# Optimization experiments

Measured on AMD Instinct MI355X. Metric: run time of the kernel, lower is better.

The kernel has to match this reference:

```python
import jax, jax.numpy as jnp
import numpy as np

NPOINT = 1024
RADIUS = 0.15
NSAMPLE = 32
BN_EPS = 1e-5


def farthest_point_sample(xyz, npoint):
    # xyz: [B, N, 3] -> idx [B, npoint]
    B, N, _ = xyz.shape

    def step(carry, _):
        dmin, far = carry
        cent = jnp.take_along_axis(xyz, far[:, None, None], axis=1)  # [B,1,3]
        d = jnp.sum((xyz - cent) ** 2, axis=-1)                      # [B,N]
        dmin = jnp.minimum(dmin, d)
        nxt = jnp.argmax(dmin, axis=-1).astype(jnp.int32)
        return (dmin, nxt), far

    init = (jnp.full((B, N), 1e10, xyz.dtype), jnp.zeros((B,), jnp.int32))
    _, idx = jax.lax.scan(step, init, None, length=npoint)
    return idx.T  # [B, npoint]


def ball_query(radius, nsample, xyz, new_xyz):
    # xyz: [B,N,3], new_xyz: [B,S,3] -> idx [B,S,nsample]
    B, S, _ = new_xyz.shape
    N = xyz.shape[1]
    sqr = jnp.sum((new_xyz[:, :, None, :] - xyz[:, None, :, :]) ** 2, axis=-1)  # [B,S,N]
    ar = jnp.broadcast_to(jnp.arange(N, dtype=jnp.int32), (B, S, N))
    gidx = jnp.where(sqr > radius * radius, N, ar)
    gidx = jnp.sort(gidx, axis=-1)[:, :, :nsample]
    first = gidx[:, :, :1]
    return jnp.where(gidx == N, first, gidx)


def setup_inputs() -> dict:
    key = jax.random.key(0)
    ks = jax.random.split(key, 8)
    B, N, Cin, Cmlp, Cout = 8, 4096, 64, 128, 256
    xyz = jax.random.uniform(ks[0], (B, N, 3), dtype=jnp.float32)
    t = jax.random.normal(ks[1], (B, 128), dtype=jnp.float32)
    points = jax.random.normal(ks[2], (B, N, Cin), dtype=jnp.float32)
    W1 = jax.random.normal(ks[3], (Cin, Cmlp), dtype=jnp.float32) / np.sqrt(Cin)
    b1 = jnp.zeros((Cmlp,), jnp.float32)
    Wc = jax.random.normal(ks[4], (Cmlp, Cout), dtype=jnp.float32) / np.sqrt(Cmlp)
    bc = jnp.zeros((Cout,), jnp.float32)
    gamma = jnp.ones((Cout,), jnp.float32)
    beta = jnp.zeros((Cout,), jnp.float32)
    return {"xyz": xyz, "t": t, "points": points, "W1": W1, "b1": b1,
            "Wc": Wc, "bc": bc, "gamma": gamma, "beta": beta}


def reference(xyz, t, points, W1, b1, Wc, bc, gamma, beta):
    # t (time embedding) is unused in the visible (truncated) forward body.
    B, N, _ = xyz.shape
    # 1) farthest point sampling -> centers
    fps_idx = farthest_point_sample(xyz, NPOINT)                     # [B,S]
    new_xyz = jnp.take_along_axis(xyz, fps_idx[:, :, None], axis=1)  # [B,S,3]
    # 2) radius ball-query grouping
    gidx = ball_query(RADIUS, NSAMPLE, xyz, new_xyz)                 # [B,S,ns]
    # 3) pointwise MLP on features, then group (gather)
    feats = points @ W1 + b1                                          # [B,N,Cmlp]
    grouped = jax.vmap(lambda f, i: f[i])(feats, gidx)                # [B,S,ns,Cmlp]
    # 4) GroupConv: 1x1 conv + BatchNorm(train stats) + ReLU
    h = jnp.einsum('bsnc,co->bsno', grouped, Wc) + bc                 # [B,S,ns,Cout]
    mean = jnp.mean(h, axis=(0, 1, 2))
    var = jnp.var(h, axis=(0, 1, 2))
    h = jax.nn.relu((h - mean) / jnp.sqrt(var + BN_EPS) * gamma + beta)
    # 5) max-pool over neighborhood
    new_points = jnp.max(h, axis=2)                                   # [B,S,Cout]
    return new_points
```

## Files before the change

### kernel.cpp

```cpp
#include <hip/hip_runtime.h>
#include <stdint.h>

#define BN 8
#define NPT 4096
#define NS 1024
#define KS 32
#define CIN 64
#define CMID 128
#define COUT 256
#define NGRP (BN*NS)

typedef short bf16x8 __attribute__((ext_vector_type(8)));
typedef float f32x4 __attribute__((ext_vector_type(4)));

__device__ __forceinline__ float bf2f(unsigned short u){
  union { unsigned int i; float f; } v; v.i = ((unsigned int)u) << 16; return v.f;
}
__device__ __forceinline__ unsigned short f2bf(float f){
  union { float f; unsigned int i; } v; v.f = f;
  unsigned int r = (v.i + 0x7fffu + ((v.i >> 16) & 1u)) >> 16;
  return (unsigned short)r;
}
__device__ __forceinline__ uint32_t pack2(float a, float b){
  return (uint32_t)f2bf(a) | ((uint32_t)f2bf(b) << 16);
}
__device__ __forceinline__ float ldf(const void* p, size_t i, bool isbf){
  return isbf ? bf2f(((const unsigned short*)p)[i]) : ((const float*)p)[i];
}
__device__ __forceinline__ bool detect_bf(const void* gamma){
  return ((const unsigned int*)gamma)[0] == 0x3F803F80u;
}

template<int CTRL>
__device__ __forceinline__ unsigned long long dpp_rot_u64(unsigned long long x){
  int lo = (int)(unsigned int)(x & 0xFFFFFFFFull);
  int hi = (int)(unsigned int)(x >> 32);
  int nlo = __builtin_amdgcn_update_dpp(0, lo, CTRL, 0xF, 0xF, true);
  int nhi = __builtin_amdgcn_update_dpp(0, hi, CTRL, 0xF, 0xF, true);
  return ((unsigned long long)(unsigned int)nhi << 32) | (unsigned int)nlo;
}
__device__ __forceinline__ unsigned long long u64max(unsigned long long a, unsigned long long b){
  return a > b ? a : b;
}

__global__ __launch_bounds__(512, 2)
void k_front(const void* __restrict__ xyz,
             const void* __restrict__ points,
             const void* __restrict__ W1,
             const void* __restrict__ Wc,
             const void* __restrict__ gamma,
             float* __restrict__ newxyz,
             unsigned short* __restrict__ featsb,
             unsigned short* __restrict__ wct,
             float* __restrict__ ps, float* __restrict__ pq, int nbins)
{
  int tid = threadIdx.x;
  int bid = blockIdx.x;
  bool isbf = detect_bf(gamma);
  __shared__ __align__(16) char smem[49152];
  __shared__ unsigned long long wk[2][8];

  if (bid < 8){
    float* sx = (float*)smem;
    float* sy = sx + NPT;
    float* sz = sy + NPT;
    size_t xb = (size_t)bid*NPT*3;
    for (int i=tid; i<NPT; i+=512){
      size_t p = xb + (size_t)i*3;
      sx[i]=ldf(xyz,p,isbf); sy[i]=ldf(xyz,p+1,isbf); sz[i]=ldf(xyz,p+2,isbf);
    }
    __syncthreads();
    int base = tid*8;
    float px0,px1,px2,px3,px4,px5,px6,px7;
    float py0,py1,py2,py3,py4,py5,py6,py7;
    float pz0,pz1,pz2,pz3,pz4,pz5,pz6,pz7;
    float dm0,dm1,dm2,dm3,dm4,dm5,dm6,dm7;
#define FPS_LOAD(k) px##k=sx[base+k]; py##k=sy[base+k]; pz##k=sz[base+k]; dm##k=1e10f;
    FPS_LOAD(0) FPS_LOAD(1) FPS_LOAD(2) FPS_LOAD(3)
    FPS_LOAD(4) FPS_LOAD(5) FPS_LOAD(6) FPS_LOAD(7)
#undef FPS_LOAD
    float cx=sx[0], cy=sy[0], cz=sz[0];
    if (tid==0){ float* o = newxyz + (size_t)bid*NS*3; o[0]=cx; o[1]=cy; o[2]=cz; }
    int lane = tid & 63, wv = tid >> 6;
    unsigned int lo0 = (unsigned int)(4095 - base);
    for (int it=1; it<NS; ++it){
      int par = it & 1;
#define FPS_STEP(k) { float dx=__fsub_rn(px##k,cx), dy=__fsub_rn(py##k,cy), dz=__fsub_rn(pz##k,cz); \
  float d=__fadd_rn(__fadd_rn(__fmul_rn(dx,dx),__fmul_rn(dy,dy)),__fmul_rn(dz,dz)); \
  dm##k=fminf(dm##k,d); }
      FPS_STEP(0) FPS_STEP(1) FPS_STEP(2) FPS_STEP(3)
      FPS_STEP(4) FPS_STEP(5) FPS_STEP(6) FPS_STEP(7)
#undef FPS_STEP
      bool c01 = dm1 > dm0; float v01 = c01?dm1:dm0; int i01 = c01?1:0;
      bool c23 = dm3 > dm2; float v23 = c23?dm3:dm2; int i23 = c23?3:2;
      bool c45 = dm5 > dm4; float v45 = c45?dm5:dm4; int i45 = c45?5:4;
      bool c67 = dm7 > dm6; float v67 = c67?dm7:dm6; int i67 = c67?7:6;
      bool ca = v23 > v01; float va = ca?v23:v01; int ia = ca?i23:i01;
      bool cb = v67 > v45; float vb = cb?v67:v45; int ib = cb?i67:i45;
      bool cc = vb  > va;  float vm = cc?vb:va;   int ir = cc?ib:ia;
      unsigned long long key =
        ((unsigned long long)__float_as_uint(vm) << 32) | (unsigned int)(lo0 - ir);
      key = u64max(key, dpp_rot_u64<0x121>(key));
      key = u64max(key, dpp_rot_u64<0x122>(key));
      key = u64max(key, dpp_rot_u64<0x124>(key));
      key = u64max(key, dpp_rot_u64<0x128>(key));
      key = u64max(key, __shfl_xor(key, 16, 64));
      key = u64max(key, __shfl_xor(key, 32, 64));
      if (lane == 0) wk[par][wv] = key;
      __syncthreads();
      const unsigned long long* w8 = wk[par];
      unsigned long long k0 =
        u64max(u64max(u64max(w8[0],w8[1]), u64max(w8[2],w8[3])),
               u64max(u64max(w8[4],w8[5]), u64max(w8[6],w8[7])));
      int widx = 4095 - (int)(k0 & 0xFFFFFFFFull);
      cx = sx[widx]; cy = sy[widx]; cz = sz[widx];
      if (tid==0){ float* o = newxyz + ((size_t)bid*NS + it)*3; o[0]=cx; o[1]=cy; o[2]=cz; }
    }
  } else if (bid == 8){
    for (int i=tid; i<CMID*COUT; i+=512){
      int k = i >> 8, n = i & 255;
      unsigned short w = isbf ? ((const unsigned short*)Wc)[i] : f2bf(((const float*)Wc)[i]);
      wct[(size_t)n*CMID + k] = w;
    }
    if (nbins != NGRP){
      for (int i=tid; i<COUT*nbins; i+=512){ ps[i]=0.f; pq[i]=0.f; }
    }
  } else {
    float* w1s = (float*)smem;
    float* pts = (float*)(smem + 32768);
    int rb = bid - 9;
    int r0g = rb*64;
    for (int i=tid; i<CIN*CMID; i+=512) w1s[i] = ldf(W1, i, isbf);
    for (int i=tid; i<64*CIN; i+=512)   pts[i] = ldf(points, (size_t)r0g*CIN + i, isbf);
    __syncthreads();
    int o0 = (tid & 15) * 8, r0 = (tid >> 4) * 2;
    float acc0[8]={0,0,0,0,0,0,0,0}, acc1[8]={0,0,0,0,0,0,0,0};
    for (int c=0;c<CIN;c++){
      float a0 = pts[r0*CIN + c], a1 = pts[(r0+1)*CIN + c];
      const float* wr = &w1s[c*CMID + o0];
      #pragma unroll
      for (int j=0;j<8;j++){ acc0[j] = fmaf(a0, wr[j], acc0[j]); acc1[j] = fmaf(a1, wr[j], acc1[j]); }
    }
    unsigned short* f0 = featsb + ((size_t)(r0g + r0))*CMID + o0;
    uint4 u;
    u.x=pack2(acc0[0],acc0[1]); u.y=pack2(acc0[2],acc0[3]); u.z=pack2(acc0[4],acc0[5]); u.w=pack2(acc0[6],acc0[7]);
    *(uint4*)f0 = u;
    u.x=pack2(acc1[0],acc1[1]); u.y=pack2(acc1[2],acc1[3]); u.z=pack2(acc1[4],acc1[5]); u.w=pack2(acc1[6],acc1[7]);
    *(uint4*)(f0 + CMID) = u;
  }
}

__global__ __launch_bounds__(256)
void k_ballq(const void* __restrict__ xyz,
             const void* __restrict__ gamma,
             const float* __restrict__ newxyz,
             int* __restrict__ gidx)
{
  __shared__ float sp[NPT*3];
  __shared__ int slots[4][KS];
  int tid = threadIdx.x;
  bool isbf = detect_bf(gamma);
  int cb = blockIdx.x * 64;
  int b = cb >> 10;
  size_t xb = (size_t)b*NPT*3;
  for (int i=tid; i<NPT*3; i+=256) sp[i] = ldf(xyz, xb + i, isbf);
  __syncthreads();
  int lane = tid & 63, wv = tid >> 6;
  const float rr = (float)(0.15*0.15);
  for (int j=0; j<16; ++j){
    int cid = cb + wv*16 + j;
    const float* cc = newxyz + (size_t)cid*3;
    float cx=cc[0], cy=cc[1], cz=cc[2];
    int cnt = 0;
    for (int ch=0; ch<64; ++ch){
      int p = ch*64 + lane;
      float dx=__fsub_rn(sp[p*3],cx), dy=__fsub_rn(sp[p*3+1],cy), dz=__fsub_rn(sp[p*3+2],cz);
      float d=__fadd_rn(__fadd_rn(__fmul_rn(dx,dx),__fmul_rn(dy,dy)),__fmul_rn(dz,dz));
      bool in = !(d > rr);
      unsigned long long mk = __ballot(in);
      int pos = cnt + __popcll(mk & ((1ull<<lane) - 1ull));
      if (in && pos < KS) slots[wv][pos] = p;
      cnt += __popcll(mk);
      if (cnt >= KS) break;
    }
    int total = cnt < KS ? cnt : KS;
    if (lane < KS){
      int v = (lane < total) ? slots[wv][lane] : slots[wv][0];
      gidx[(size_t)cid*KS + lane] = v;
    }
  }
}

__global__ __launch_bounds__(256)
void k_group(const unsigned short* __restrict__ featsb,
             const unsigned short* __restrict__ wct,
             const int* __restrict__ gidx,
             const void* __restrict__ gamma,
             float* __restrict__ ps, float* __restrict__ pq,
             const float* __restrict__ av, const float* __restrict__ cv,
             float* __restrict__ hM,
             void* __restrict__ out, int mode, int nbins)
{
  int tid = threadIdx.x;
  int bs  = blockIdx.x;
  __shared__ unsigned short g[32][136];
  __shared__ int gi[KS];
  if (tid < KS) gi[tid] = gidx[(size_t)bs*KS + tid];
  __syncthreads();
  {
    int r = tid >> 3, sg = tid & 7;
    const unsigned short* src = featsb + ((size_t)(bs>>10)*NPT + gi[r])*CMID + sg*16;
    uint4 v0 = *(const uint4*)src;
    uint4 v1 = *(const uint4*)(src + 8);
    *(uint4*)(&g[r][sg*16])     = v0;
    *(uint4*)(&g[r][sg*16 + 8]) = v1;
  }
  __syncthreads();
  int lane = tid & 63, wv = tid >> 6;
  int m = lane & 15, quad = lane >> 4;
  f32x4 acc[2][4];
  #pragma unroll
  for (int a=0;a<2;a++)
    #pragma unroll
    for (int b2=0;b2<4;b2++) acc[a][b2] = (f32x4){0.f,0.f,0.f,0.f};
  int n0 = wv * 64;
  #pragma unroll
  for (int k0=0; k0<CMID; k0+=32){
    bf16x8 a0 = *(const bf16x8*)(&g[m][k0 + quad*8]);
    bf16x8 a1 = *(const bf16x8*)(&g[16 + m][k0 + quad*8]);
    #pragma unroll
    for (int nt=0; nt<4; nt++){
      int n = n0 + nt*16 + m;
      bf16x8 bb = *(const bf16x8*)(wct + (size_t)n*CMID + k0 + quad*8);
      acc[0][nt] = __builtin_amdgcn_mfma_f32_16x16x32_bf16(a0, bb, acc[0][nt], 0, 0, 0);
      acc[1][nt] = __builtin_amdgcn_mfma_f32_16x16x32_bf16(a1, bb, acc[1][nt], 0, 0, 0);
    }
  }
  if (mode == 2){
    #pragma unroll
    for (int nt=0; nt<4; nt++){
      float s=0.f, q=0.f, hx=-3.402823466e38f;
      #pragma unroll
      for (int mt=0; mt<2; mt++)
        #pragma unroll
        for (int rg=0; rg<4; rg++){ float h = acc[mt][nt][rg]; s += h; q += h*h; hx = fmaxf(hx,h); }
      s += __shfl_xor(s,16,64); q += __shfl_xor(q,16,64); hx = fmaxf(hx, __shfl_xor(hx,16,64));
      s += __shfl_xor(s,32,64); q += __shfl_xor(q,32,64); hx = fmaxf(hx, __shfl_xor(hx,32,64));
      if (quad == 0){
        int o = n0 + nt*16 + m;
        ps[(size_t)o*NGRP + bs] = s;
        pq[(size_t)o*NGRP + bs] = q;
        hM[(size_t)bs*COUT + o] = hx;
      }
    }
  } else if (mode == 0){
    #pragma unroll
    for (int nt=0; nt<4; nt++){
      float s=0.f, q=0.f;
      #pragma unroll
      for (int mt=0; mt<2; mt++)
        #pragma unroll
        for (int rg=0; rg<4; rg++){ float h = acc[mt][nt][rg]; s += h; q += h*h; }
      s += __shfl_xor(s,16,64); q += __shfl_xor(q,16,64);
      s += __shfl_xor(s,32,64); q += __shfl_xor(q,32,64);
      if (quad == 0){
        int o = n0 + nt*16 + m;
        atomicAdd(&ps[(size_t)o*nbins + (bs & (nbins-1))], s);
        atomicAdd(&pq[(size_t)o*nbins + (bs & (nbins-1))], q);
      }
    }
  } else {
    bool isbf = detect_bf(gamma);
    #pragma unroll
    for (int nt=0; nt<4; nt++){
      int o = n0 + nt*16 + m;
      float a = av[o], c = cv[o];
      float v = 0.f;
      #pragma unroll
      for (int mt=0; mt<2; mt++)
        #pragma unroll
        for (int rg=0; rg<4; rg++){ v = fmaxf(v, acc[mt][nt][rg]*a + c); }
      v = fmaxf(v, __shfl_xor(v,16,64));
      v = fmaxf(v, __shfl_xor(v,32,64));
      if (quad == 0){
        size_t oi = (size_t)bs*COUT + o;
        if (isbf) ((unsigned short*)out)[oi] = f2bf(v);
        else      ((float*)out)[oi] = v;
      }
    }
  }
}

__global__ __launch_bounds__(256)
void k_bnprep(const float* __restrict__ ps, const float* __restrict__ pq,
              const void* __restrict__ gamma, const void* __restrict__ beta,
              float* __restrict__ av, float* __restrict__ cv, int nbins)
{
  int tid = threadIdx.x, o = blockIdx.x;
  bool isbf = detect_bf(gamma);
  float s=0.f, q=0.f;
  for (int i=tid; i<nbins; i+=256){ s += ps[(size_t)o*nbins + i]; q += pq[(size_t)o*nbins + i]; }
  #pragma unroll
  for (int off=1; off<64; off<<=1){ s += __shfl_xor(s,off,64); q += __shfl_xor(q,off,64); }
  __shared__ float ls[4], lq[4];
  int lane = tid & 63, wv = tid >> 6;
  if (lane == 0){ ls[wv]=s; lq[wv]=q; }
  __syncthreads();
  if (tid == 0){
    float S = ls[0]+ls[1]+ls[2]+ls[3], Q = lq[0]+lq[1]+lq[2]+lq[3];
    const float invM = 1.0f/262144.0f;
    float mean = S*invM;
    float var  = fmaxf(Q*invM - mean*mean, 0.f);
    float inv  = 1.0f/sqrtf(var + 1e-5f);
    float a = ldf(gamma,o,isbf)*inv;
    float c = ldf(beta,o,isbf) - mean*a;
    av[o]=a; cv[o]=c;
  }
}

__global__ __launch_bounds__(256)
void k_bnfinal(const float* __restrict__ hM,
               const float* __restrict__ av, const float* __restrict__ cv,
               const void* __restrict__ gamma, void* __restrict__ out)
{
  int idx = blockIdx.x*256 + threadIdx.x;
  int o = idx & 255;
  float a = av[o], c = cv[o];
  float v = fmaxf(hM[idx]*a + c, 0.f);
  if (detect_bf(gamma)) ((unsigned short*)out)[idx] = f2bf(v);
  else                  ((float*)out)[idx] = v;
}

extern "C" void kernel_launch(void* const* d_in, const int* in_sizes, int n_in,
                              void* d_out, int out_size, void* d_ws, size_t ws_size,
                              hipStream_t stream)
{
  const void* xyz    = d_in[0];
  const void* points = d_in[2];
  const void* W1     = d_in[3];
  const void* Wc     = d_in[5];
  const void* gamma  = d_in[7];
  const void* beta   = d_in[8];

  char* ws = (char*)d_ws;
  unsigned short* featsb = (unsigned short*)(ws + 0);
  unsigned short* wct    = (unsigned short*)(ws + 8388608);
  float* newxyz          = (float*)(ws + 8454144);
  int*   gidx            = (int*)(ws + 8552448);
  float* ps              = (float*)(ws + 9601024);
  bool bigws = ws_size >= (size_t)34768896;
  int nbins = bigws ? NGRP : 64;
  float* pq = ps + (size_t)COUT*nbins;
  float* av = pq + (size_t)COUT*nbins;
  float* cv = av + COUT;
  float* hM = (float*)(ws + 26380288);

  hipLaunchKernelGGL(k_front,  dim3(521), dim3(512), 0, stream,
                     xyz, points, W1, Wc, gamma, newxyz, featsb, wct, ps, pq, nbins);
  hipLaunchKernelGGL(k_ballq,  dim3(128), dim3(256), 0, stream, xyz, gamma, newxyz, gidx);
  if (bigws){
    hipLaunchKernelGGL(k_group,  dim3(8192), dim3(256), 0, stream,
                       featsb, wct, gidx, gamma, ps, pq, av, cv, hM, d_out, 2, nbins);
    hipLaunchKernelGGL(k_bnprep, dim3(256),  dim3(256), 0, stream, ps, pq, gamma, beta, av, cv, nbins);
    hipLaunchKernelGGL(k_bnfinal,dim3(8192), dim3(256), 0, stream, hM, av, cv, gamma, d_out);
  } else {
    hipLaunchKernelGGL(k_group,  dim3(8192), dim3(256), 0, stream,
                       featsb, wct, gidx, gamma, ps, pq, av, cv, hM, d_out, 0, nbins);
    hipLaunchKernelGGL(k_bnprep, dim3(256),  dim3(256), 0, stream, ps, pq, gamma, beta, av, cv, nbins);
    hipLaunchKernelGGL(k_group,  dim3(8192), dim3(256), 0, stream,
                       featsb, wct, gidx, gamma, ps, pq, av, cv, hM, d_out, 1, nbins);
  }
}
```

Measured before the change: 1.055 ms.

## Morton-sort points in FPS and skip waves whose bounding box cannot change

The FPS block now bins its points by a coarse Morton code, using a shared-memory histogram and prefix scan, so each wave holds a spatially compact cluster. Before each iteration a wave checks whether the new center's distance to its bounding box can lower any of its current min-distances, and skips the distance update and reduction when it cannot. The argmax key carries the original index so ties still resolve the same way. The BN statistics path is unified into a single k_group pass that atomically accumulates into 512 bins and writes max-h, replacing the workspace-size-dependent two-pass fallback. It adds sort overhead and more shared memory, and the skip test uses a 0.999 slack factor that could affect exactness.

```diff
diff --git a/kernel.cpp b/kernel.cpp
--- a/kernel.cpp
+++ b/kernel.cpp
@@ -8,10 +8,11 @@
 #define CIN 64
 #define CMID 128
 #define COUT 256
-#define NGRP (BN*NS)
+#define NBINS 512
 
 typedef short bf16x8 __attribute__((ext_vector_type(8)));
 typedef float f32x4 __attribute__((ext_vector_type(4)));
+typedef unsigned long long u64;
 
 __device__ __forceinline__ float bf2f(unsigned short u){
   union { unsigned int i; float f; } v; v.i = ((unsigned int)u) << 16; return v.f;
@@ -30,20 +31,27 @@
 __device__ __forceinline__ bool detect_bf(const void* gamma){
   return ((const unsigned int*)gamma)[0] == 0x3F803F80u;
 }
-
 template<int CTRL>
-__device__ __forceinline__ unsigned long long dpp_rot_u64(unsigned long long x){
+__device__ __forceinline__ u64 dpp_rot_u64(u64 x){
   int lo = (int)(unsigned int)(x & 0xFFFFFFFFull);
   int hi = (int)(unsigned int)(x >> 32);
   int nlo = __builtin_amdgcn_update_dpp(0, lo, CTRL, 0xF, 0xF, true);
   int nhi = __builtin_amdgcn_update_dpp(0, hi, CTRL, 0xF, 0xF, true);
-  return ((unsigned long long)(unsigned int)nhi << 32) | (unsigned int)nlo;
-}
-__device__ __forceinline__ unsigned long long u64max(unsigned long long a, unsigned long long b){
-  return a > b ? a : b;
-}
-
-__global__ __launch_bounds__(512, 2)
+  return ((u64)(unsigned int)nhi << 32) | (unsigned int)nlo;
+}
+__device__ __forceinline__ u64 u64max(u64 a, u64 b){ return a > b ? a : b; }
+
+__device__ __forceinline__ unsigned mcode(float x, float y, float z){
+  int ix = (int)(x*16.f); ix = ix<0?0:(ix>15?15:ix);
+  int iy = (int)(y*16.f); iy = iy<0?0:(iy>15?15:iy);
+  int iz = (int)(z*8.f);  iz = iz<0?0:(iz>7?7:iz);
+  return ((unsigned)(iy&1))      | ((unsigned)(ix&1)<<1) | ((unsigned)(iz&1)<<2)
+       | ((unsigned)(iy&2)<<2)   | ((unsigned)(ix&2)<<3) | ((unsigned)(iz&2)<<4)
+       | ((unsigned)(iy&4)<<4)   | ((unsigned)(ix&4)<<5) | ((unsigned)(iz&4)<<6)
+       | ((unsigned)(iy&8)<<6)   | ((unsigned)(ix&8)<<7);
+}
+
+__global__ __launch_bounds__(512, 4)
 void k_front(const void* __restrict__ xyz,
              const void* __restrict__ points,
              const void* __restrict__ W1,
@@ -52,68 +60,113 @@
              float* __restrict__ newxyz,
              unsigned short* __restrict__ featsb,
              unsigned short* __restrict__ wct,
-             float* __restrict__ ps, float* __restrict__ pq, int nbins)
+             float* __restrict__ ps, float* __restrict__ pq)
 {
   int tid = threadIdx.x;
   int bid = blockIdx.x;
   bool isbf = detect_bf(gamma);
-  __shared__ __align__(16) char smem[49152];
-  __shared__ unsigned long long wk[2][8];
+  __shared__ __align__(16) char smem[65536];
+  __shared__ unsigned tsum[512];
+  __shared__ u64 wk[2][8];
 
   if (bid < 8){
-    float* sx = (float*)smem;
-    float* sy = sx + NPT;
-    float* sz = sy + NPT;
+    float* ssx = (float*)smem;
+    float* ssy = ssx + NPT;
+    float* ssz = ssy + NPT;
+    unsigned short* snl = (unsigned short*)(ssz + NPT);
+    unsigned* hist = (unsigned*)(smem + 57344);
     size_t xb = (size_t)bid*NPT*3;
-    for (int i=tid; i<NPT; i+=512){
-      size_t p = xb + (size_t)i*3;
-      sx[i]=ldf(xyz,p,isbf); sy[i]=ldf(xyz,p+1,isbf); sz[i]=ldf(xyz,p+2,isbf);
-    }
-    __syncthreads();
     int base = tid*8;
-    float px0,px1,px2,px3,px4,px5,px6,px7;
-    float py0,py1,py2,py3,py4,py5,py6,py7;
-    float pz0,pz1,pz2,pz3,pz4,pz5,pz6,pz7;
-    float dm0,dm1,dm2,dm3,dm4,dm5,dm6,dm7;
-#define FPS_LOAD(k) px##k=sx[base+k]; py##k=sy[base+k]; pz##k=sz[base+k]; dm##k=1e10f;
-    FPS_LOAD(0) FPS_LOAD(1) FPS_LOAD(2) FPS_LOAD(3)
-    FPS_LOAD(4) FPS_LOAD(5) FPS_LOAD(6) FPS_LOAD(7)
-#undef FPS_LOAD
-    float cx=sx[0], cy=sy[0], cz=sz[0];
+    for (int i=tid; i<2048; i+=512) hist[i]=0;
+    __syncthreads();
+    unsigned codes[8];
+    #pragma unroll
+    for (int k=0;k<8;k++){
+      size_t p = xb + (size_t)(base+k)*3;
+      unsigned c = mcode(ldf(xyz,p,isbf), ldf(xyz,p+1,isbf), ldf(xyz,p+2,isbf));
+      codes[k]=c;
+      atomicAdd(&hist[c],1u);
+    }
+    __syncthreads();
+    unsigned l0=hist[tid*4],l1=hist[tid*4+1],l2=hist[tid*4+2],l3=hist[tid*4+3];
+    unsigned s = l0+l1+l2+l3;
+    tsum[tid]=s; __syncthreads();
+    for (int off=1; off<512; off<<=1){
+      unsigned v = (tid>=off)? tsum[tid-off]:0u; __syncthreads();
+      tsum[tid]+=v; __syncthreads();
+    }
+    unsigned ex = tsum[tid]-s;
+    hist[tid*4]=ex; hist[tid*4+1]=ex+l0; hist[tid*4+2]=ex+l0+l1; hist[tid*4+3]=ex+l0+l1+l2;
+    __syncthreads();
+    #pragma unroll
+    for (int k=0;k<8;k++){
+      size_t p = xb + (size_t)(base+k)*3;
+      float x=ldf(xyz,p,isbf), y=ldf(xyz,p+1,isbf), z=ldf(xyz,p+2,isbf);
+      unsigned pos = atomicAdd(&hist[codes[k]],1u);
+      ssx[pos]=x; ssy[pos]=y; ssz[pos]=z; snl[pos]=(unsigned short)(4095-(base+k));
+    }
+    __syncthreads();
+    float qx0,qx1,qx2,qx3,qx4,qx5,qx6,qx7;
+    float qy0,qy1,qy2,qy3,qy4,qy5,qy6,qy7;
+    float qz0,qz1,qz2,qz3,qz4,qz5,qz6,qz7;
+    float dd0,dd1,dd2,dd3,dd4,dd5,dd6,dd7;
+    unsigned lk0,lk1,lk2,lk3,lk4,lk5,lk6,lk7;
+#define LOADS(k) { int p=base+k; qx##k=ssx[p]; qy##k=ssy[p]; qz##k=ssz[p]; dd##k=1e10f; \
+  lk##k = ((unsigned)snl[p]<<12) | (unsigned)p; }
+    LOADS(0) LOADS(1) LOADS(2) LOADS(3) LOADS(4) LOADS(5) LOADS(6) LOADS(7)
+#undef LOADS
+    float bxl = fminf(fminf(fminf(qx0,qx1),fminf(qx2,qx3)),fminf(fminf(qx4,qx5),fminf(qx6,qx7)));
+    float bxh = fmaxf(fmaxf(fmaxf(qx0,qx1),fmaxf(qx2,qx3)),fmaxf(fmaxf(qx4,qx5),fmaxf(qx6,qx7)));
+    float byl = fminf(fminf(fminf(qy0,qy1),fminf(qy2,qy3)),fminf(fminf(qy4,qy5),fminf(qy6,qy7)));
+    float byh = fmaxf(fmaxf(fmaxf(qy0,qy1),fmaxf(qy2,qy3)),fmaxf(fmaxf(qy4,qy5),fmaxf(qy6,qy7)));
+    float bzl = fminf(fminf(fminf(qz0,qz1),fminf(qz2,qz3)),fminf(fminf(qz4,qz5),fminf(qz6,qz7)));
+    float bzh = fmaxf(fmaxf(fmaxf(qz0,qz1),fmaxf(qz2,qz3)),fmaxf(fmaxf(qz4,qz5),fmaxf(qz6,qz7)));
+    #pragma unroll
+    for (int off=1; off<64; off<<=1){
+      bxl = fminf(bxl, __shfl_xor(bxl,off,64)); bxh = fmaxf(bxh, __shfl_xor(bxh,off,64));
+      byl = fminf(byl, __shfl_xor(byl,off,64)); byh = fmaxf(byh, __shfl_xor(byh,off,64));
+      bzl = fminf(bzl, __shfl_xor(bzl,off,64)); bzh = fmaxf(bzh, __shfl_xor(bzh,off,64));
+    }
+    float cx=ldf(xyz,xb,isbf), cy=ldf(xyz,xb+1,isbf), cz=ldf(xyz,xb+2,isbf);
     if (tid==0){ float* o = newxyz + (size_t)bid*NS*3; o[0]=cx; o[1]=cy; o[2]=cz; }
     int lane = tid & 63, wv = tid >> 6;
-    unsigned int lo0 = (unsigned int)(4095 - base);
+    u64 ckey = ((u64)__float_as_uint(1e10f) << 32);
     for (int it=1; it<NS; ++it){
       int par = it & 1;
-#define FPS_STEP(k) { float dx=__fsub_rn(px##k,cx), dy=__fsub_rn(py##k,cy), dz=__fsub_rn(pz##k,cz); \
+      float ex2 = fmaxf(fmaxf(__fsub_rn(bxl,cx), __fsub_rn(cx,bxh)), 0.f);
+      float ey2 = fmaxf(fmaxf(__fsub_rn(byl,cy), __fsub_rn(cy,byh)), 0.f);
+      float ez2 = fmaxf(fmaxf(__fsub_rn(bzl,cz), __fsub_rn(cz,bzh)), 0.f);
+      float lb2 = ex2*ex2 + ey2*ey2 + ez2*ez2;
+      float wtmax = __uint_as_float((unsigned)(ckey >> 32));
+      bool act = !(lb2*0.999f >= wtmax);
+      if (__builtin_amdgcn_readfirstlane((int)act)){
+#define FPS_STEP(k) { float dx=__fsub_rn(qx##k,cx), dy=__fsub_rn(qy##k,cy), dz=__fsub_rn(qz##k,cz); \
   float d=__fadd_rn(__fadd_rn(__fmul_rn(dx,dx),__fmul_rn(dy,dy)),__fmul_rn(dz,dz)); \
-  dm##k=fminf(dm##k,d); }
-      FPS_STEP(0) FPS_STEP(1) FPS_STEP(2) FPS_STEP(3)
-      FPS_STEP(4) FPS_STEP(5) FPS_STEP(6) FPS_STEP(7)
+  dd##k=fminf(dd##k,d); }
+        FPS_STEP(0) FPS_STEP(1) FPS_STEP(2) FPS_STEP(3)
+        FPS_STEP(4) FPS_STEP(5) FPS_STEP(6) FPS_STEP(7)
 #undef FPS_STEP
-      bool c01 = dm1 > dm0; float v01 = c01?dm1:dm0; int i01 = c01?1:0;
-      bool c23 = dm3 > dm2; float v23 = c23?dm3:dm2; int i23 = c23?3:2;
-      bool c45 = dm5 > dm4; float v45 = c45?dm5:dm4; int i45 = c45?5:4;
-      bool c67 = dm7 > dm6; float v67 = c67?dm7:dm6; int i67 = c67?7:6;
-      bool ca = v23 > v01; float va = ca?v23:v01; int ia = ca?i23:i01;
-      bool cb = v67 > v45; float vb = cb?v67:v45; int ib = cb?i67:i45;
-      bool cc = vb  > va;  float vm = cc?vb:va;   int ir = cc?ib:ia;
-      unsigned long long key =
-        ((unsigned long long)__float_as_uint(vm) << 32) | (unsigned int)(lo0 - ir);
-      key = u64max(key, dpp_rot_u64<0x121>(key));
-      key = u64max(key, dpp_rot_u64<0x122>(key));
-      key = u64max(key, dpp_rot_u64<0x124>(key));
-      key = u64max(key, dpp_rot_u64<0x128>(key));
-      key = u64max(key, __shfl_xor(key, 16, 64));
-      key = u64max(key, __shfl_xor(key, 32, 64));
-      if (lane == 0) wk[par][wv] = key;
+#define KEYK(k) ( ((u64)__float_as_uint(dd##k) << 32) | lk##k )
+        u64 e0=u64max(KEYK(0),KEYK(1)), e2=u64max(KEYK(2),KEYK(3));
+        u64 e4=u64max(KEYK(4),KEYK(5)), e6=u64max(KEYK(6),KEYK(7));
+#undef KEYK
+        e0=u64max(e0,e2); e4=u64max(e4,e6);
+        u64 key=u64max(e0,e4);
+        key = u64max(key, dpp_rot_u64<0x121>(key));
+        key = u64max(key, dpp_rot_u64<0x122>(key));
+        key = u64max(key, dpp_rot_u64<0x124>(key));
+        key = u64max(key, dpp_rot_u64<0x128>(key));
+        key = u64max(key, __shfl_xor(key, 16, 64));
+        key = u64max(key, __shfl_xor(key, 32, 64));
+        ckey = key;
+      }
+      if (lane == 0) wk[par][wv] = ckey;
       __syncthreads();
-      const unsigned long long* w8 = wk[par];
-      unsigned long long k0 =
-        u64max(u64max(u64max(w8[0],w8[1]), u64max(w8[2],w8[3])),
-               u64max(u64max(w8[4],w8[5]), u64max(w8[6],w8[7])));
-      int widx = 4095 - (int)(k0 & 0xFFFFFFFFull);
-      cx = sx[widx]; cy = sy[widx]; cz = sz[widx];
+      const u64* w8 = wk[par];
+      u64 k0 = u64max(u64max(u64max(w8[0],w8[1]), u64max(w8[2],w8[3])),
+                      u64max(u64max(w8[4],w8[5]), u64max(w8[6],w8[7])));
+      unsigned spos = (unsigned)(k0 & 0xFFFu);
+      cx = ssx[spos]; cy = ssy[spos]; cz = ssz[spos];
       if (tid==0){ float* o = newxyz + ((size_t)bid*NS + it)*3; o[0]=cx; o[1]=cy; o[2]=cz; }
     }
   } else if (bid == 8){
@@ -122,9 +175,7 @@
       unsigned short w = isbf ? ((const unsigned short*)Wc)[i] : f2bf(((const float*)Wc)[i]);
       wct[(size_t)n*CMID + k] = w;
     }
-    if (nbins != NGRP){
-      for (int i=tid; i<COUT*nbins; i+=512){ ps[i]=0.f; pq[i]=0.f; }
-    }
+    for (int i=tid; i<COUT*NBINS; i+=512){ ps[i]=0.f; pq[i]=0.f; }
   } else {
     float* w1s = (float*)smem;
     float* pts = (float*)(smem + 32768);
@@ -177,7 +228,7 @@
       float dx=__fsub_rn(sp[p*3],cx), dy=__fsub_rn(sp[p*3+1],cy), dz=__fsub_rn(sp[p*3+2],cz);
       float d=__fadd_rn(__fadd_rn(__fmul_rn(dx,dx),__fmul_rn(dy,dy)),__fmul_rn(dz,dz));
       bool in = !(d > rr);
-      unsigned long long mk = __ballot(in);
+      u64 mk = __ballot(in);
       int pos = cnt + __popcll(mk & ((1ull<<lane) - 1ull));
       if (in && pos < KS) slots[wv][pos] = p;
       cnt += __popcll(mk);
@@ -195,11 +246,8 @@
 void k_group(const unsigned short* __restrict__ featsb,
              const unsigned short* __restrict__ wct,
              const int* __restrict__ gidx,
-             const void* __restrict__ gamma,
              float* __restrict__ ps, float* __restrict__ pq,
-             const float* __restrict__ av, const float* __restrict__ cv,
-             float* __restrict__ hM,
-             void* __restrict__ out, int mode, int nbins)
+             float* __restrict__ hM)
 {
   int tid = threadIdx.x;
   int bs  = blockIdx.x;
@@ -236,57 +284,21 @@
       acc[1][nt] = __builtin_amdgcn_mfma_f32_16x16x32_bf16(a1, bb, acc[1][nt], 0, 0, 0);
     }
   }
-  if (mode == 2){
-    #pragma unroll
-    for (int nt=0; nt<4; nt++){
-      float s=0.f, q=0.f, hx=-3.402823466e38f;
+  int bin = bs & (NBINS-1);
+  #pragma unroll
+  for (int nt=0; nt<4; nt++){
+    float s=0.f, q=0.f, hx=-3.402823466e38f;
+    #pragma unroll
+    for (int mt=0; mt<2; mt++)
       #pragma unroll
-      for (int mt=0; mt<2; mt++)
-        #pragma unroll
-        for (int rg=0; rg<4; rg++){ float h = acc[mt][nt][rg]; s += h; q += h*h; hx = fmaxf(hx,h); }
-      s += __shfl_xor(s,16,64); q += __shfl_xor(q,16,64); hx = fmaxf(hx, __shfl_xor(hx,16,64));
-      s += __shfl_xor(s,32,64); q += __shfl_xor(q,32,64); hx = fmaxf(hx, __shfl_xor(hx,32,64));
-      if (quad == 0){
-        int o = n0 + nt*16 + m;
-        ps[(size_t)o*NGRP + bs] = s;
-        pq[(size_t)o*NGRP + bs] = q;
-        hM[(size_t)bs*COUT + o] = hx;
-      }
-    }
-  } else if (mode == 0){
-    #pragma unroll
-    for (int nt=0; nt<4; nt++){
-      float s=0.f, q=0.f;
-      #pragma unroll
-      for (int mt=0; mt<2; mt++)
-        #pragma unroll
-        for (int rg=0; rg<4; rg++){ float h = acc[mt][nt][rg]; s += h; q += h*h; }
-      s += __shfl_xor(s,16,64); q += __shfl_xor(q,16,64);
-      s += __shfl_xor(s,32,64); q += __shfl_xor(q,32,64);
-      if (quad == 0){
-        int o = n0 + nt*16 + m;
-        atomicAdd(&ps[(size_t)o*nbins + (bs & (nbins-1))], s);
-        atomicAdd(&pq[(size_t)o*nbins + (bs & (nbins-1))], q);
-      }
-    }
-  } else {
-    bool isbf = detect_bf(gamma);
-    #pragma unroll
-    for (int nt=0; nt<4; nt++){
+      for (int rg=0; rg<4; rg++){ float h = acc[mt][nt][rg]; s += h; q += h*h; hx = fmaxf(hx,h); }
+    s += __shfl_xor(s,16,64); q += __shfl_xor(q,16,64); hx = fmaxf(hx, __shfl_xor(hx,16,64));
+    s += __shfl_xor(s,32,64); q += __shfl_xor(q,32,64); hx = fmaxf(hx, __shfl_xor(hx,32,64));
+    if (quad == 0){
       int o = n0 + nt*16 + m;
-      float a = av[o], c = cv[o];
-      float v = 0.f;
-      #pragma unroll
-      for (int mt=0; mt<2; mt++)
-        #pragma unroll
-        for (int rg=0; rg<4; rg++){ v = fmaxf(v, acc[mt][nt][rg]*a + c); }
-      v = fmaxf(v, __shfl_xor(v,16,64));
-      v = fmaxf(v, __shfl_xor(v,32,64));
-      if (quad == 0){
-        size_t oi = (size_t)bs*COUT + o;
-        if (isbf) ((unsigned short*)out)[oi] = f2bf(v);
-        else      ((float*)out)[oi] = v;
-      }
+      atomicAdd(&ps[(size_t)o*NBINS + bin], s);
+      atomicAdd(&pq[(size_t)o*NBINS + bin], q);
+      hM[(size_t)bs*COUT + o] = hx;
     }
   }
 }
@@ -294,12 +306,12 @@
 __global__ __launch_bounds__(256)
 void k_bnprep(const float* __restrict__ ps, const float* __restrict__ pq,
               const void* __restrict__ gamma, const void* __restrict__ beta,
-              float* __restrict__ av, float* __restrict__ cv, int nbins)
+              float* __restrict__ av, float* __restrict__ cv)
 {
   int tid = threadIdx.x, o = blockIdx.x;
   bool isbf = detect_bf(gamma);
   float s=0.f, q=0.f;
-  for (int i=tid; i<nbins; i+=256){ s += ps[(size_t)o*nbins + i]; q += pq[(size_t)o*nbins + i]; }
+  for (int i=tid; i<NBINS; i+=256){ s += ps[(size_t)o*NBINS + i]; q += pq[(size_t)o*NBINS + i]; }
   #pragma unroll
   for (int off=1; off<64; off<<=1){ s += __shfl_xor(s,off,64); q += __shfl_xor(q,off,64); }
   __shared__ float ls[4], lq[4];
@@ -325,8 +337,7 @@
 {
   int idx = blockIdx.x*256 + threadIdx.x;
   int o = idx & 255;
-  float a = av[o], c = cv[o];
-  float v = fmaxf(hM[idx]*a + c, 0.f);
+  float v = fmaxf(hM[idx]*av[o] + cv[o], 0.f);
   if (detect_bf(gamma)) ((unsigned short*)out)[idx] = f2bf(v);
   else                  ((float*)out)[idx] = v;
 }
@@ -347,27 +358,17 @@
   unsigned short* wct    = (unsigned short*)(ws + 8388608);
   float* newxyz          = (float*)(ws + 8454144);
   int*   gidx            = (int*)(ws + 8552448);
-  float* ps              = (float*)(ws + 9601024);
-  bool bigws = ws_size >= (size_t)34768896;
-  int nbins = bigws ? NGRP : 64;
-  float* pq = ps + (size_t)COUT*nbins;
-  float* av = pq + (size_t)COUT*nbins;
-  float* cv = av + COUT;
-  float* hM = (float*)(ws + 26380288);
+  float* hM              = (float*)(ws + 9601024);
+  float* ps              = (float*)(ws + 17989632);
+  float* pq              = (float*)(ws + 18513920);
+  float* av              = (float*)(ws + 19038208);
+  float* cv              = (float*)(ws + 19039232);
 
   hipLaunchKernelGGL(k_front,  dim3(521), dim3(512), 0, stream,
-                     xyz, points, W1, Wc, gamma, newxyz, featsb, wct, ps, pq, nbins);
+                     xyz, points, W1, Wc, gamma, newxyz, featsb, wct, ps, pq);
   hipLaunchKernelGGL(k_ballq,  dim3(128), dim3(256), 0, stream, xyz, gamma, newxyz, gidx);
-  if (bigws){
-    hipLaunchKernelGGL(k_group,  dim3(8192), dim3(256), 0, stream,
-                       featsb, wct, gidx, gamma, ps, pq, av, cv, hM, d_out, 2, nbins);
-    hipLaunchKernelGGL(k_bnprep, dim3(256),  dim3(256), 0, stream, ps, pq, gamma, beta, av, cv, nbins);
-    hipLaunchKernelGGL(k_bnfinal,dim3(8192), dim3(256), 0, stream, hM, av, cv, gamma, d_out);
-  } else {
-    hipLaunchKernelGGL(k_group,  dim3(8192), dim3(256), 0, stream,
-                       featsb, wct, gidx, gamma, ps, pq, av, cv, hM, d_out, 0, nbins);
-    hipLaunchKernelGGL(k_bnprep, dim3(256),  dim3(256), 0, stream, ps, pq, gamma, beta, av, cv, nbins);
-    hipLaunchKernelGGL(k_group,  dim3(8192), dim3(256), 0, stream,
-                       featsb, wct, gidx, gamma, ps, pq, av, cv, hM, d_out, 1, nbins);
-  }
-}
+  hipLaunchKernelGGL(k_group,  dim3(8192), dim3(256), 0, stream,
+                     featsb, wct, gidx, ps, pq, hM);
+  hipLaunchKernelGGL(k_bnprep, dim3(256),  dim3(256), 0, stream, ps, pq, gamma, beta, av, cv);
+  hipLaunchKernelGGL(k_bnfinal,dim3(8192), dim3(256), 0, stream, hM, av, cv, gamma, d_out);
+}
```

After: 1.102 ms. +4.5%, slower.
